# Kernel optimization log

Hardware: AMD Instinct MI355X
Metric: run time of the kernel (lower is better)

The kernel has to match this reference:

```python
import jax, jax.numpy as jnp
import numpy as np

B, N, C_IN = 16, 4096, 64
NPOINT = 1024
RADII = (0.2, 0.4)
NSAMPLES = (32, 64)
MLPS = ((64, 64, 128), (64, 64, 128))
C_TOTAL = sum(m[-1] for m in MLPS)


def setup_inputs() -> dict:
    key = jax.random.key(0)
    ks = jax.random.split(key, 24)
    inp = {
        "xyz": jax.random.uniform(ks[0], (B, N, 3), jnp.float32),
        "features": jax.random.normal(ks[1], (B, N, C_IN), jnp.float32),
        "w_att": jax.random.normal(ks[2], (3 * NPOINT, C_TOTAL), jnp.float32) * 0.02,
        "b_att": jnp.zeros((C_TOTAL,), jnp.float32),
    }
    k = 3
    for g, mlp in enumerate(MLPS):
        cin = 3 + C_IN
        for l, cout in enumerate(mlp):
            inp[f"w{g}_{l}"] = jax.random.normal(ks[k], (cout, cin), jnp.float32) * (1.0 / np.sqrt(cin))
            inp[f"b{g}_{l}"] = jnp.zeros((cout,), jnp.float32)
            k += 1
            cin = cout
    return inp


def _fps(xyz, npoint):
    # furthest point sampling; xyz (B,N,3) -> idx (B,npoint) int32. First idx is 0 (matches CUDA op).
    b, n, _ = xyz.shape
    init_idx = jnp.zeros((b,), jnp.int32)
    init_dist = jnp.full((b, n), 1e10, xyz.dtype)

    def body(carry, _):
        dists, last = carry
        last_pt = jnp.take_along_axis(xyz, last[:, None, None].astype(jnp.int32), axis=1)  # (B,1,3)
        d = jnp.sum((xyz - last_pt) ** 2, axis=-1)  # (B,N)
        dists = jnp.minimum(dists, d)
        nxt = jnp.argmax(dists, axis=-1).astype(jnp.int32)
        return (dists, nxt), nxt

    (_, _), rest = jax.lax.scan(body, (init_dist, init_idx), None, length=npoint - 1)
    return jnp.concatenate([init_idx[None, :], rest], axis=0).T  # (B, npoint)


def _ball_query(radius, nsample, xyz, new_xyz):
    # first-nsample points of xyz within radius of each new_xyz center (slots padded with first hit)
    n = xyz.shape[1]
    d2 = jnp.sum((new_xyz[:, :, None, :] - xyz[:, None, :, :]) ** 2, axis=-1)  # (B,S,N)
    mask = d2 < radius * radius
    order_key = jnp.where(mask, jnp.arange(n, dtype=jnp.int32)[None, None, :], n)
    idx = jnp.argsort(order_key, axis=-1)[..., :nsample].astype(jnp.int32)  # (B,S,nsample)
    valid = jnp.take_along_axis(mask, idx, axis=-1)
    return jnp.where(valid, idx, idx[..., :1])


def _group(xyz, new_xyz, features, idx):
    # -> (B, 3+C, S, nsample): relative xyz concat grouped features
    b, s, ns = idx.shape
    flat = idx.reshape(b, s * ns)
    gx = jnp.take_along_axis(xyz, flat[..., None], axis=1).reshape(b, s, ns, 3)
    gx = gx - new_xyz[:, :, None, :]
    gf = jnp.take_along_axis(features, flat[..., None], axis=1).reshape(b, s, ns, features.shape[-1])
    return jnp.transpose(jnp.concatenate([gx, gf], axis=-1), (0, 3, 1, 2))


def reference(xyz, features, w_att, b_att,
              w0_0, b0_0, w0_1, b0_1, w0_2, b0_2,
              w1_0, b1_0, w1_1, b1_1, w1_2, b1_2):
    xyz_sg = jax.lax.stop_gradient(xyz)  # index selection is non-differentiable (matches CUDA ops)
    fps_idx = _fps(xyz_sg, NPOINT)  # (B, npoint)
    new_xyz = jnp.take_along_axis(xyz, fps_idx[..., None], axis=1)  # (B, npoint, 3)

    # attention gate from sampled coordinates: (B, 3, npoint) flattened -> (B, C_TOTAL)
    att_in = jnp.transpose(new_xyz, (0, 2, 1)).reshape(xyz.shape[0], 3 * NPOINT)
    att = jax.nn.sigmoid(att_in @ w_att + b_att)  # (B, C_TOTAL)

    layer_sets = (((w0_0, b0_0), (w0_1, b0_1), (w0_2, b0_2)),
                  ((w1_0, b1_0), (w1_1, b1_1), (w1_2, b1_2)))
    pooled = []
    new_xyz_sg = jax.lax.stop_gradient(new_xyz)
    for radius, ns, layers in zip(RADII, NSAMPLES, layer_sets):
        idx = _ball_query(radius, ns, xyz_sg, new_xyz_sg)
        x = _group(xyz, new_xyz, features, idx)  # (B, 3+C, S, ns)
        for w, b in layers:  # shared 1x1 conv + ReLU per layer
            x = jax.nn.relu(jnp.einsum('oc,bcsn->bosn', w, x) + b[None, :, None, None])
        pooled.append(jnp.max(x, axis=-1))  # max over nsample -> (B, cout, S)

    features_cat = jnp.concatenate(pooled, axis=1)  # (B, C_TOTAL, S)
    features_end = features_cat * att[:, :, None]
    return new_xyz, features_end
```

## Files before the change

### kernel.cpp

```cpp
#include <hip/hip_runtime.h>
#include <cstdint>
#include <cstddef>


constexpr int B_ = 16, N_ = 4096, S_ = 1024;
constexpr int WT_G = 67*64 + 64*64 + 128*64 + 64 + 64 + 128;
constexpr int WT_BLK = (2*WT_G + 255) / 256;
constexpr int G1_BLK = 2 * B_ * (N_ / 256);

constexpr int WS_XYZF = 0;
constexpr int WS_NXYZ = B_*N_*4;
constexpr int WS_ATT  = WS_NXYZ + B_*S_*3;
constexpr int WS_WT   = WS_ATT + B_*256;
constexpr int WS_IDX0 = WS_WT + 2*WT_G;
constexpr int WS_IDX1 = WS_IDX0 + B_*S_*32;
constexpr int WS_F1   = WS_IDX1 + B_*S_*64;

__global__ __launch_bounds__(256) void g1_kernel(
    const float* __restrict__ xyz, const float* __restrict__ feats,
    const float* __restrict__ w00, const float* __restrict__ w10,
    float* __restrict__ f1) {
  __shared__ float wfs[67 * 64];
  const int fid = blockIdx.x;
  const int g = fid >> 8, b = (fid >> 4) & 15, chunk = fid & 15;
  const float* w = g ? w10 : w00;
  for (int k = threadIdx.x; k < 67*64; k += 256) {
    int c = k >> 6, o = k & 63;
    wfs[k] = w[o*67 + c];
  }
  __syncthreads();
  const int p = chunk * 256 + threadIdx.x;
  const float* xr = xyz + ((size_t)b * N_ + p) * 3;
  const float* fr = feats + ((size_t)b * N_ + p) * 64;
  float acc[64];
  {
    float x0 = xr[0], x1 = xr[1], x2 = xr[2];
#pragma unroll
    for (int j = 0; j < 64; j += 4) {
      float4 wA = *(const float4*)&wfs[0*64 + j];
      acc[j+0] = wA.x * x0; acc[j+1] = wA.y * x0;
      acc[j+2] = wA.z * x0; acc[j+3] = wA.w * x0;
    }
#pragma unroll
    for (int j = 0; j < 64; j += 4) {
      float4 wA = *(const float4*)&wfs[1*64 + j];
      acc[j+0] = fmaf(wA.x, x1, acc[j+0]); acc[j+1] = fmaf(wA.y, x1, acc[j+1]);
      acc[j+2] = fmaf(wA.z, x1, acc[j+2]); acc[j+3] = fmaf(wA.w, x1, acc[j+3]);
    }
#pragma unroll
    for (int j = 0; j < 64; j += 4) {
      float4 wA = *(const float4*)&wfs[2*64 + j];
      acc[j+0] = fmaf(wA.x, x2, acc[j+0]); acc[j+1] = fmaf(wA.y, x2, acc[j+1]);
      acc[j+2] = fmaf(wA.z, x2, acc[j+2]); acc[j+3] = fmaf(wA.w, x2, acc[j+3]);
    }
  }
  for (int c = 0; c < 64; ++c) {
    float v = fr[c];
    const float* wr = &wfs[(3 + c) * 64];
#pragma unroll
    for (int j = 0; j < 64; j += 4) {
      float4 w4 = *(const float4*)&wr[j];
      acc[j+0] = fmaf(w4.x, v, acc[j+0]); acc[j+1] = fmaf(w4.y, v, acc[j+1]);
      acc[j+2] = fmaf(w4.z, v, acc[j+2]); acc[j+3] = fmaf(w4.w, v, acc[j+3]);
    }
  }
  float* op = f1 + (((size_t)g * B_ + b) * N_ + p) * 64;
#pragma unroll
  for (int j = 0; j < 64; j += 4) {
    float4 r = make_float4(acc[j], acc[j+1], acc[j+2], acc[j+3]);
    *(float4*)&op[j] = r;
  }
}

__global__ __launch_bounds__(256) void fps_wt_kernel(
    const float* __restrict__ xyz,
    const float* __restrict__ w00, const float* __restrict__ w01,
    const float* __restrict__ w02, const float* __restrict__ b00,
    const float* __restrict__ b01, const float* __restrict__ b02,
    const float* __restrict__ w10, const float* __restrict__ w11,
    const float* __restrict__ w12, const float* __restrict__ b10,
    const float* __restrict__ b11, const float* __restrict__ b12,
    float4* __restrict__ xyzf, float* __restrict__ wt,
    float* __restrict__ nxyz, float* __restrict__ out_nxyz) {
  constexpr int PPT = 16;
  __shared__ float sx[N_*3];
  __shared__ int   selidx[S_];
  __shared__ alignas(16) unsigned long long redP[2][4];
  __shared__ alignas(16) float4 redC[2][4];

  if (blockIdx.x >= B_) {
    int wid = (blockIdx.x - B_) * 256 + threadIdx.x;
    if (wid >= 2*WT_G) return;
    int g = wid / WT_G, r = wid % WT_G;
    float val;
    if (r < 4288) {
      int c = r >> 6, o = r & 63;
      val = (g ? w10 : w00)[o*67 + c];
    } else if (r < 8384) {
      int rr = r - 4288; int c = rr >> 6, o = rr & 63;
      val = (g ? w11 : w01)[o*64 + c];
    } else if (r < 16576) {
      int rr = r - 8384; int c = rr >> 7, o = rr & 127;
      val = (g ? w12 : w02)[o*64 + c];
    } else {
      int rr = r - 16576;
      val = (rr < 64)  ? (g ? b10 : b00)[rr]
          : (rr < 128) ? (g ? b11 : b01)[rr - 64]
                       : (g ? b12 : b02)[rr - 128];
    }
    wt[g*WT_G + r] = val;
    return;
  }

  const int b = blockIdx.x, t = threadIdx.x;
  const int wv = t >> 6;
  const float* xr = xyz + (size_t)b * N_ * 3;
  for (int k = t; k < N_*3; k += 256) sx[k] = xr[k];
  if (t == 0) selidx[0] = 0;
  __syncthreads();
  float px[PPT], py[PPT], pz[PPT], m[PPT];
#pragma unroll
  for (int p = 0; p < PPT; ++p) {
    int idx = t * PPT + p;
    px[p] = sx[idx*3+0]; py[p] = sx[idx*3+1]; pz[p] = sx[idx*3+2];
    m[p] = 1e10f;
  }
  float lx = sx[0], ly = sx[1], lz = sx[2];
  for (int i = 1; i < S_; ++i) {
#pragma unroll
    for (int p = 0; p < PPT; ++p) {
      float dx = __fsub_rn(px[p], lx), dy = __fsub_rn(py[p], ly), dz = __fsub_rn(pz[p], lz);
      float d = __fadd_rn(__fadd_rn(__fmul_rn(dx,dx), __fmul_rn(dy,dy)), __fmul_rn(dz,dz));
      m[p] = fminf(m[p], d);
    }
    float h0 = fmaxf(fmaxf(m[0],  m[1]),  fmaxf(m[2],  m[3]));
    float h1 = fmaxf(fmaxf(m[4],  m[5]),  fmaxf(m[6],  m[7]));
    float h2 = fmaxf(fmaxf(m[8],  m[9]),  fmaxf(m[10], m[11]));
    float h3 = fmaxf(fmaxf(m[12], m[13]), fmaxf(m[14], m[15]));
    float bv = fmaxf(fmaxf(h0, h1), fmaxf(h2, h3));
    int bp = PPT - 1;
#pragma unroll
    for (int p = PPT - 2; p >= 0; --p)
      if (m[p] == bv) bp = p;
    const int bi = t * PPT + bp;
    unsigned vm = __float_as_uint(bv);
#define DPP_MAX(ctrl) { unsigned o = (unsigned)__builtin_amdgcn_update_dpp((int)vm, (int)vm, (ctrl), 0xf, 0xf, false); vm = vm > o ? vm : o; }
    DPP_MAX(0x111)
    DPP_MAX(0x112)
    DPP_MAX(0x114)
    DPP_MAX(0x118)
    DPP_MAX(0x142)
    DPP_MAX(0x143)
#undef DPP_MAX
    const unsigned wmaxu = (unsigned)__builtin_amdgcn_readlane((int)vm, 63);
    const unsigned long long mk = __ballot(__float_as_uint(bv) == wmaxu);
    const int fl = (int)__builtin_ctzll(mk);
    const int widx = __builtin_amdgcn_readlane(bi, fl);
    const int par = i & 1;
    if (t == (widx >> 4)) {
      const int psel = widx & 15;
      float gx = px[0], gy = py[0], gz = pz[0];
#pragma unroll
      for (int p = 1; p < PPT; ++p)
        if (psel == p) { gx = px[p]; gy = py[p]; gz = pz[p]; }
      redP[par][wv] = ((unsigned long long)wmaxu << 32) | (unsigned)(~widx);
      redC[par][wv] = make_float4(gx, gy, gz, 0.f);
    }
    __syncthreads();
    ulonglong2 pA = *(const ulonglong2*)&redP[par][0];
    ulonglong2 pB = *(const ulonglong2*)&redP[par][2];
    float4 c0 = redC[par][0], c1 = redC[par][1];
    float4 c2 = redC[par][2], c3 = redC[par][3];
    unsigned long long q0 = pA.x > pA.y ? pA.x : pA.y;
    unsigned long long q1 = pB.x > pB.y ? pB.x : pB.y;
    unsigned long long win = q0 > q1 ? q0 : q1;
    const int fi = (int)(~(unsigned)win);
    const int ws = fi >> 10;
    float4 s0 = (ws & 1) ? c1 : c0;
    float4 s1 = (ws & 1) ? c3 : c2;
    float4 fc = (ws & 2) ? s1 : s0;
    lx = fc.x; ly = fc.y; lz = fc.z;
    if (t == 0) selidx[i] = fi;
  }
  __syncthreads();
  for (int k = t; k < S_; k += 256) {
    int id = selidx[k];
    float x = sx[id*3], y = sx[id*3+1], z = sx[id*3+2];
    int o = (b * S_ + k) * 3;
    nxyz[o] = x; nxyz[o+1] = y; nxyz[o+2] = z;
    out_nxyz[o] = x; out_nxyz[o+1] = y; out_nxyz[o+2] = z;
  }
  for (int k = t; k < N_; k += 256) {
    float4 v; v.x = sx[k*3]; v.y = sx[k*3+1]; v.z = sx[k*3+2]; v.w = 0.f;
    xyzf[b * N_ + k] = v;
  }
}

__global__ __launch_bounds__(256) void ballq_att_kernel(
    const float4* __restrict__ xyzf, const float* __restrict__ nxyz,
    int* __restrict__ idx0buf, int* __restrict__ idx1buf,
    const float* __restrict__ w_att, const float* __restrict__ b_att,
    float* __restrict__ att) {
  __shared__ float ai[3 * S_];
  if (blockIdx.x >= B_*S_/4) {
    int b = blockIdx.x - B_*S_/4, t = threadIdx.x;
    for (int k = t; k < 3 * S_; k += 256) {
      int d = k >> 10, s = k & 1023;
      ai[k] = nxyz[(b * S_ + s) * 3 + d];
    }
    __syncthreads();
    float acc = b_att[t];
#pragma unroll 8
    for (int k = 0; k < 3 * S_; ++k)
      acc = fmaf(ai[k], w_att[k * 256 + t], acc);
    att[b * 256 + t] = 1.f / (1.f + expf(-acc));
    return;
  }
  const float r2a = (float)(0.2 * 0.2), r2b = (float)(0.4 * 0.4);
  int lane = threadIdx.x & 63;
  int cid = blockIdx.x * 4 + (threadIdx.x >> 6);
  int b = cid >> 10;
  float cx = nxyz[cid*3], cy = nxyz[cid*3+1], cz = nxyz[cid*3+2];
  const float4* xb = xyzf + b * N_;
  int cnt0 = 0, cnt1 = 0, first0 = 0, first1 = 0;
  const unsigned long long below = (1ull << lane) - 1ull;
  for (int base = 0; base < N_; base += 64) {
    float4 P = xb[base + lane];
    float dx = __fsub_rn(cx, P.x), dy = __fsub_rn(cy, P.y), dz = __fsub_rn(cz, P.z);
    float d2 = __fadd_rn(__fadd_rn(__fmul_rn(dx,dx), __fmul_rn(dy,dy)), __fmul_rn(dz,dz));
    bool h0 = d2 < r2a, h1 = d2 < r2b;
    unsigned long long m0 = __ballot(h0), m1 = __ballot(h1);
    if (cnt0 == 0 && m0 != 0ull) first0 = base + (int)__builtin_ctzll(m0);
    if (cnt1 == 0 && m1 != 0ull) first1 = base + (int)__builtin_ctzll(m1);
    if (h0) {
      int pos = cnt0 + (int)__popcll(m0 & below);
      if (pos < 32) idx0buf[cid * 32 + pos] = base + lane;
    }
    if (h1) {
      int pos = cnt1 + (int)__popcll(m1 & below);
      if (pos < 64) idx1buf[cid * 64 + pos] = base + lane;
    }
    cnt0 += (int)__popcll(m0);
    cnt1 += (int)__popcll(m1);
    if (cnt0 >= 32 && cnt1 >= 64) break;
  }
  if (cnt0 < 32)
    for (int p = cnt0 + lane; p < 32; p += 64) idx0buf[cid * 32 + p] = first0;
  if (cnt1 < 64)
    for (int p = cnt1 + lane; p < 64; p += 64) idx1buf[cid * 64 + p] = first1;
}

template<int NS>
__device__ __forceinline__ void mlp_body(int bi, float* xs, int* pidx,
    float* c1s, const float* __restrict__ f1g,
    const float* __restrict__ nxyz, const float* __restrict__ att,
    const int* __restrict__ idxbuf, const float* __restrict__ wt,
    float* __restrict__ outf, int g) {
  constexpr int NCEN = 128 / NS;
  constexpr int XS = 132;
  float* red = xs;
  const int t = threadIdx.x;
  const int cid0 = bi * NCEN;
  const int b = cid0 >> 10;

  const float* w0  = wt;
  const float* w1  = wt + 67*64;
  const float* w2  = w1 + 64*64;
  const float* bb0 = w2 + 64*128;
  const float* bb1 = bb0 + 64;
  const float* bb2 = bb1 + 64;

  if (t < 128) {
    const int col = t;
    const int cidg = cid0 + col / NS;
    pidx[col] = idxbuf[cidg * NS + (col % NS)];
  }
  if (t < 64 * NCEN) {
    const int o = t & 63, ci = t >> 6;
    const int cid = cid0 + ci;
    float nx = nxyz[cid*3], ny = nxyz[cid*3+1], nz = nxyz[cid*3+2];
    c1s[ci*64 + o] = fmaf(w0[128+o], nz, fmaf(w0[64+o], ny, w0[o]*nx));
  }
  __syncthreads();

  const int og = t & 15, cg = t >> 4;
  float acc[4][8];

  {
    float4 bv = *(const float4*)&bb0[og*4];
    const int ctr = (cg * 8) / NS;
    float4 cv = *(const float4*)&c1s[ctr*64 + og*4];
    float bc[4] = {bv.x - cv.x, bv.y - cv.y, bv.z - cv.z, bv.w - cv.w};
    const int4 pA = *(const int4*)&pidx[cg*8];
    const int4 pB = *(const int4*)&pidx[cg*8 + 4];
    int pc[8] = {pA.x, pA.y, pA.z, pA.w, pB.x, pB.y, pB.z, pB.w};
#pragma unroll
    for (int cc = 0; cc < 8; ++cc) {
      float4 fv = *(const float4*)&f1g[((size_t)b * N_ + pc[cc]) * 64 + og*4];
      acc[0][cc] = bc[0] + fv.x;
      acc[1][cc] = bc[1] + fv.y;
      acc[2][cc] = bc[2] + fv.z;
      acc[3][cc] = bc[3] + fv.w;
    }
  }
#pragma unroll
  for (int oo = 0; oo < 4; ++oo) {
    float4 y0, y1;
    y0.x=fmaxf(acc[oo][0],0.f); y0.y=fmaxf(acc[oo][1],0.f);
    y0.z=fmaxf(acc[oo][2],0.f); y0.w=fmaxf(acc[oo][3],0.f);
    y1.x=fmaxf(acc[oo][4],0.f); y1.y=fmaxf(acc[oo][5],0.f);
    y1.z=fmaxf(acc[oo][6],0.f); y1.w=fmaxf(acc[oo][7],0.f);
    *(float4*)&xs[(og*4+oo)*XS + cg*8]     = y0;
    *(float4*)&xs[(og*4+oo)*XS + cg*8 + 4] = y1;
  }
  __syncthreads();

  {
    float4 bv = *(const float4*)&bb1[og*4];
    float b4[4] = {bv.x, bv.y, bv.z, bv.w};
#pragma unroll
    for (int oo = 0; oo < 4; ++oo)
#pragma unroll
      for (int cc = 0; cc < 8; ++cc) acc[oo][cc] = b4[oo];
    for (int k = 0; k < 64; ++k) {
      float4 x0 = *(const float4*)&xs[k*XS + cg*8];
      float4 x1 = *(const float4*)&xs[k*XS + cg*8 + 4];
      float4 wv = *(const float4*)&w1[k*64 + og*4];
      float x8[8] = {x0.x,x0.y,x0.z,x0.w,x1.x,x1.y,x1.z,x1.w};
      float w4[4] = {wv.x,wv.y,wv.z,wv.w};
#pragma unroll
      for (int oo = 0; oo < 4; ++oo)
#pragma unroll
        for (int cc = 0; cc < 8; ++cc) acc[oo][cc] = fmaf(w4[oo], x8[cc], acc[oo][cc]);
    }
  }
  __syncthreads();
#pragma unroll
  for (int oo = 0; oo < 4; ++oo) {
    float4 y0, y1;
    y0.x=fmaxf(acc[oo][0],0.f); y0.y=fmaxf(acc[oo][1],0.f);
    y0.z=fmaxf(acc[oo][2],0.f); y0.w=fmaxf(acc[oo][3],0.f);
    y1.x=fmaxf(acc[oo][4],0.f); y1.y=fmaxf(acc[oo][5],0.f);
    y1.z=fmaxf(acc[oo][6],0.f); y1.w=fmaxf(acc[oo][7],0.f);
    *(float4*)&xs[(og*4+oo)*XS + cg*8]     = y0;
    *(float4*)&xs[(og*4+oo)*XS + cg*8 + 4] = y1;
  }
  __syncthreads();

  float acc3[8][8];
  {
    float4 b0v = *(const float4*)&bb2[og*8];
    float4 b1v = *(const float4*)&bb2[og*8 + 4];
    float b8[8] = {b0v.x,b0v.y,b0v.z,b0v.w,b1v.x,b1v.y,b1v.z,b1v.w};
#pragma unroll
    for (int oo = 0; oo < 8; ++oo)
#pragma unroll
      for (int cc = 0; cc < 8; ++cc) acc3[oo][cc] = b8[oo];
    for (int k = 0; k < 64; ++k) {
      float4 x0 = *(const float4*)&xs[k*XS + cg*8];
      float4 x1 = *(const float4*)&xs[k*XS + cg*8 + 4];
      float4 wa = *(const float4*)&w2[k*128 + og*8];
      float4 wb = *(const float4*)&w2[k*128 + og*8 + 4];
      float x8[8] = {x0.x,x0.y,x0.z,x0.w,x1.x,x1.y,x1.z,x1.w};
      float w8[8] = {wa.x,wa.y,wa.z,wa.w,wb.x,wb.y,wb.z,wb.w};
#pragma unroll
      for (int oo = 0; oo < 8; ++oo)
#pragma unroll
        for (int cc = 0; cc < 8; ++cc) acc3[oo][cc] = fmaf(w8[oo], x8[cc], acc3[oo][cc]);
    }
  }
  float pm[8];
#pragma unroll
  for (int oo = 0; oo < 8; ++oo) {
    float v = fmaxf(acc3[oo][0], 0.f);
#pragma unroll
    for (int cc = 1; cc < 8; ++cc) v = fmaxf(v, fmaxf(acc3[oo][cc], 0.f));
    pm[oo] = v;
  }
#pragma unroll
  for (int oo = 0; oo < 8; ++oo) {
    pm[oo] = fmaxf(pm[oo], __shfl_xor(pm[oo], 16));
    pm[oo] = fmaxf(pm[oo], __shfl_xor(pm[oo], 32));
  }
  __syncthreads();
  if ((t & 63) < 16) {
    int w = t >> 6;
#pragma unroll
    for (int oo = 0; oo < 8; ++oo) red[w*128 + og*8 + oo] = pm[oo];
  }
  __syncthreads();

  const int ch = t & 127;
  const float a = att[b*256 + g*128 + ch];
  if (NS == 64) {
    int c = t >> 7;
    float v = fmaxf(red[(2*c)*128 + ch], red[(2*c+1)*128 + ch]);
    int s = (cid0 + c) & 1023;
    outf[((size_t)(b*256 + g*128 + ch)) * 1024 + s] = v * a;
  } else {
#pragma unroll
    for (int kk = 0; kk < 2; ++kk) {
      int c = (t >> 7) * 2 + kk;
      float v = red[c*128 + ch];
      int s = (cid0 + c) & 1023;
      outf[((size_t)(b*256 + g*128 + ch)) * 1024 + s] = v * a;
    }
  }
}

__global__ __launch_bounds__(256, 4) void mlp_kernel(
    const float* __restrict__ f1, const float* __restrict__ nxyz,
    const float* __restrict__ att, const int* __restrict__ idx0,
    const int* __restrict__ idx1, const float* __restrict__ wt,
    float* __restrict__ outf) {
  constexpr int XS = 132;
  __shared__ float xs[64 * XS];
  __shared__ int pidx[128];
  __shared__ float c1s[256];
  if (blockIdx.x < 4096)
    mlp_body<32>(blockIdx.x, xs, pidx, c1s, f1, nxyz, att, idx0, wt, outf, 0);
  else
    mlp_body<64>(blockIdx.x - 4096, xs, pidx, c1s, f1 + (size_t)B_*N_*64,
                 nxyz, att, idx1, wt + WT_G, outf, 1);
}

extern "C" void kernel_launch(void* const* d_in, const int* in_sizes, int n_in,
                              void* d_out, int out_size, void* d_ws, size_t ws_size,
                              hipStream_t stream) {
  const float* xyz   = (const float*)d_in[0];
  const float* feats = (const float*)d_in[1];
  const float* w_att = (const float*)d_in[2];
  const float* b_att = (const float*)d_in[3];
  const float* w00 = (const float*)d_in[4];
  const float* b00 = (const float*)d_in[5];
  const float* w01 = (const float*)d_in[6];
  const float* b01 = (const float*)d_in[7];
  const float* w02 = (const float*)d_in[8];
  const float* b02 = (const float*)d_in[9];
  const float* w10 = (const float*)d_in[10];
  const float* b10 = (const float*)d_in[11];
  const float* w11 = (const float*)d_in[12];
  const float* b11 = (const float*)d_in[13];
  const float* w12 = (const float*)d_in[14];
  const float* b12 = (const float*)d_in[15];

  float* wsf = (float*)d_ws;
  int*   wsi = (int*)d_ws;
  float4* xyzf = (float4*)(wsf + WS_XYZF);
  float* nxyz  = wsf + WS_NXYZ;
  float* att   = wsf + WS_ATT;
  float* wt    = wsf + WS_WT;
  int* idx0 = wsi + WS_IDX0;
  int* idx1 = wsi + WS_IDX1;
  float* f1 = wsf + WS_F1;

  float* out  = (float*)d_out;
  float* outf = out + B_ * S_ * 3;

  hipLaunchKernelGGL(g1_kernel, dim3(G1_BLK), dim3(256), 0, stream,
                     xyz, feats, w00, w10, f1);
  hipLaunchKernelGGL(fps_wt_kernel, dim3(B_ + WT_BLK), dim3(256), 0, stream,
                     xyz, w00, w01, w02, b00, b01, b02, w10, w11, w12,
                     b10, b11, b12, xyzf, wt, nxyz, out);
  hipLaunchKernelGGL(ballq_att_kernel, dim3(B_*S_/4 + B_), dim3(256), 0, stream,
                     xyzf, nxyz, idx0, idx1, w_att, b_att, att);
  hipLaunchKernelGGL(mlp_kernel, dim3(12288), dim3(256), 0, stream,
                     f1, nxyz, att, idx0, idx1, wt, outf);
}
```

Baseline: 1.587 ms.

## Process two batches per FPS block to interleave independent serial chains

The furthest point sampling kernel now handles two batch elements per block, with separate shared buffers and register sets, and interleaves their distance updates, DPP reductions and cross-wave reductions so both share one barrier per iteration. The goal is to hide the latency of the serial per-iteration reduction and barrier chain by giving each wave two independent instruction streams. In exchange it doubles register and LDS use per block (about 96KB of shared coordinates) and halves the number of FPS blocks, which lowers parallelism across CUs and may reduce occupancy.

```diff
diff --git a/kernel.cpp b/kernel.cpp
--- a/kernel.cpp
+++ b/kernel.cpp
@@ -7,6 +7,7 @@
 constexpr int WT_G = 67*64 + 64*64 + 128*64 + 64 + 64 + 128;
 constexpr int WT_BLK = (2*WT_G + 255) / 256;
 constexpr int G1_BLK = 2 * B_ * (N_ / 256);
+constexpr int FPB = B_ / 2;
 
 constexpr int WS_XYZF = 0;
 constexpr int WS_NXYZ = B_*N_*4;
@@ -83,13 +84,15 @@
     float4* __restrict__ xyzf, float* __restrict__ wt,
     float* __restrict__ nxyz, float* __restrict__ out_nxyz) {
   constexpr int PPT = 16;
-  __shared__ float sx[N_*3];
-  __shared__ int   selidx[S_];
-  __shared__ alignas(16) unsigned long long redP[2][4];
-  __shared__ alignas(16) float4 redC[2][4];
-
-  if (blockIdx.x >= B_) {
-    int wid = (blockIdx.x - B_) * 256 + threadIdx.x;
+  __shared__ float sxA[N_*3];
+  __shared__ float sxB[N_*3];
+  __shared__ int   selidxA[S_];
+  __shared__ int   selidxB[S_];
+  __shared__ alignas(16) unsigned long long redP[2][2][4];
+  __shared__ alignas(16) float4 redC[2][2][4];
+
+  if (blockIdx.x >= FPB) {
+    int wid = (blockIdx.x - FPB) * 256 + threadIdx.x;
     if (wid >= 2*WT_G) return;
     int g = wid / WT_G, r = wid % WT_G;
     float val;
@@ -112,87 +115,145 @@
     return;
   }
 
-  const int b = blockIdx.x, t = threadIdx.x;
+  const int bA = blockIdx.x, bB = blockIdx.x + FPB, t = threadIdx.x;
   const int wv = t >> 6;
-  const float* xr = xyz + (size_t)b * N_ * 3;
-  for (int k = t; k < N_*3; k += 256) sx[k] = xr[k];
-  if (t == 0) selidx[0] = 0;
-  __syncthreads();
-  float px[PPT], py[PPT], pz[PPT], m[PPT];
+  {
+    const float* xrA = xyz + (size_t)bA * N_ * 3;
+    const float* xrB = xyz + (size_t)bB * N_ * 3;
+    for (int k = t; k < N_*3; k += 256) { sxA[k] = xrA[k]; sxB[k] = xrB[k]; }
+  }
+  if (t == 0) { selidxA[0] = 0; selidxB[0] = 0; }
+  __syncthreads();
+  float pxA[PPT], pyA[PPT], pzA[PPT], mA[PPT];
+  float pxB[PPT], pyB[PPT], pzB[PPT], mB[PPT];
 #pragma unroll
   for (int p = 0; p < PPT; ++p) {
     int idx = t * PPT + p;
-    px[p] = sx[idx*3+0]; py[p] = sx[idx*3+1]; pz[p] = sx[idx*3+2];
-    m[p] = 1e10f;
-  }
-  float lx = sx[0], ly = sx[1], lz = sx[2];
+    pxA[p] = sxA[idx*3+0]; pyA[p] = sxA[idx*3+1]; pzA[p] = sxA[idx*3+2];
+    pxB[p] = sxB[idx*3+0]; pyB[p] = sxB[idx*3+1]; pzB[p] = sxB[idx*3+2];
+    mA[p] = 1e10f; mB[p] = 1e10f;
+  }
+  float lxA = sxA[0], lyA = sxA[1], lzA = sxA[2];
+  float lxB = sxB[0], lyB = sxB[1], lzB = sxB[2];
+
+#define DPP_STEP(v, ctrl) { unsigned o_ = (unsigned)__builtin_amdgcn_update_dpp((int)(v), (int)(v), (ctrl), 0xf, 0xf, false); (v) = (v) > o_ ? (v) : o_; }
+
   for (int i = 1; i < S_; ++i) {
 #pragma unroll
     for (int p = 0; p < PPT; ++p) {
-      float dx = __fsub_rn(px[p], lx), dy = __fsub_rn(py[p], ly), dz = __fsub_rn(pz[p], lz);
+      float dx = __fsub_rn(pxA[p], lxA), dy = __fsub_rn(pyA[p], lyA), dz = __fsub_rn(pzA[p], lzA);
       float d = __fadd_rn(__fadd_rn(__fmul_rn(dx,dx), __fmul_rn(dy,dy)), __fmul_rn(dz,dz));
-      m[p] = fminf(m[p], d);
-    }
-    float h0 = fmaxf(fmaxf(m[0],  m[1]),  fmaxf(m[2],  m[3]));
-    float h1 = fmaxf(fmaxf(m[4],  m[5]),  fmaxf(m[6],  m[7]));
-    float h2 = fmaxf(fmaxf(m[8],  m[9]),  fmaxf(m[10], m[11]));
-    float h3 = fmaxf(fmaxf(m[12], m[13]), fmaxf(m[14], m[15]));
-    float bv = fmaxf(fmaxf(h0, h1), fmaxf(h2, h3));
-    int bp = PPT - 1;
+      mA[p] = fminf(mA[p], d);
+    }
+#pragma unroll
+    for (int p = 0; p < PPT; ++p) {
+      float dx = __fsub_rn(pxB[p], lxB), dy = __fsub_rn(pyB[p], lyB), dz = __fsub_rn(pzB[p], lzB);
+      float d = __fadd_rn(__fadd_rn(__fmul_rn(dx,dx), __fmul_rn(dy,dy)), __fmul_rn(dz,dz));
+      mB[p] = fminf(mB[p], d);
+    }
+    float hA0 = fmaxf(fmaxf(mA[0],  mA[1]),  fmaxf(mA[2],  mA[3]));
+    float hA1 = fmaxf(fmaxf(mA[4],  mA[5]),  fmaxf(mA[6],  mA[7]));
+    float hA2 = fmaxf(fmaxf(mA[8],  mA[9]),  fmaxf(mA[10], mA[11]));
+    float hA3 = fmaxf(fmaxf(mA[12], mA[13]), fmaxf(mA[14], mA[15]));
+    float bvA = fmaxf(fmaxf(hA0, hA1), fmaxf(hA2, hA3));
+    int bpA = PPT - 1;
 #pragma unroll
     for (int p = PPT - 2; p >= 0; --p)
-      if (m[p] == bv) bp = p;
-    const int bi = t * PPT + bp;
-    unsigned vm = __float_as_uint(bv);
-#define DPP_MAX(ctrl) { unsigned o = (unsigned)__builtin_amdgcn_update_dpp((int)vm, (int)vm, (ctrl), 0xf, 0xf, false); vm = vm > o ? vm : o; }
-    DPP_MAX(0x111)
-    DPP_MAX(0x112)
-    DPP_MAX(0x114)
-    DPP_MAX(0x118)
-    DPP_MAX(0x142)
-    DPP_MAX(0x143)
-#undef DPP_MAX
-    const unsigned wmaxu = (unsigned)__builtin_amdgcn_readlane((int)vm, 63);
-    const unsigned long long mk = __ballot(__float_as_uint(bv) == wmaxu);
-    const int fl = (int)__builtin_ctzll(mk);
-    const int widx = __builtin_amdgcn_readlane(bi, fl);
+      if (mA[p] == bvA) bpA = p;
+    const int biA = t * PPT + bpA;
+    float hB0 = fmaxf(fmaxf(mB[0],  mB[1]),  fmaxf(mB[2],  mB[3]));
+    float hB1 = fmaxf(fmaxf(mB[4],  mB[5]),  fmaxf(mB[6],  mB[7]));
+    float hB2 = fmaxf(fmaxf(mB[8],  mB[9]),  fmaxf(mB[10], mB[11]));
+    float hB3 = fmaxf(fmaxf(mB[12], mB[13]), fmaxf(mB[14], mB[15]));
+    float bvB = fmaxf(fmaxf(hB0, hB1), fmaxf(hB2, hB3));
+    int bpB = PPT - 1;
+#pragma unroll
+    for (int p = PPT - 2; p >= 0; --p)
+      if (mB[p] == bvB) bpB = p;
+    const int biB = t * PPT + bpB;
+    unsigned vmA = __float_as_uint(bvA);
+    unsigned vmB = __float_as_uint(bvB);
+    DPP_STEP(vmA, 0x111) DPP_STEP(vmB, 0x111)
+    DPP_STEP(vmA, 0x112) DPP_STEP(vmB, 0x112)
+    DPP_STEP(vmA, 0x114) DPP_STEP(vmB, 0x114)
+    DPP_STEP(vmA, 0x118) DPP_STEP(vmB, 0x118)
+    DPP_STEP(vmA, 0x142) DPP_STEP(vmB, 0x142)
+    DPP_STEP(vmA, 0x143) DPP_STEP(vmB, 0x143)
+    const unsigned wmaxuA = (unsigned)__builtin_amdgcn_readlane((int)vmA, 63);
+    const unsigned wmaxuB = (unsigned)__builtin_amdgcn_readlane((int)vmB, 63);
+    const unsigned long long mkA = __ballot(__float_as_uint(bvA) == wmaxuA);
+    const unsigned long long mkB = __ballot(__float_as_uint(bvB) == wmaxuB);
+    const int flA = (int)__builtin_ctzll(mkA);
+    const int flB = (int)__builtin_ctzll(mkB);
+    const int widxA = __builtin_amdgcn_readlane(biA, flA);
+    const int widxB = __builtin_amdgcn_readlane(biB, flB);
     const int par = i & 1;
-    if (t == (widx >> 4)) {
-      const int psel = widx & 15;
-      float gx = px[0], gy = py[0], gz = pz[0];
+    if (t == (widxA >> 4)) {
+      const int psel = widxA & 15;
+      float gx = pxA[0], gy = pyA[0], gz = pzA[0];
 #pragma unroll
       for (int p = 1; p < PPT; ++p)
-        if (psel == p) { gx = px[p]; gy = py[p]; gz = pz[p]; }
-      redP[par][wv] = ((unsigned long long)wmaxu << 32) | (unsigned)(~widx);
-      redC[par][wv] = make_float4(gx, gy, gz, 0.f);
+        if (psel == p) { gx = pxA[p]; gy = pyA[p]; gz = pzA[p]; }
+      redP[0][par][wv] = ((unsigned long long)wmaxuA << 32) | (unsigned)(~widxA);
+      redC[0][par][wv] = make_float4(gx, gy, gz, 0.f);
+    }
+    if (t == (widxB >> 4)) {
+      const int psel = widxB & 15;
+      float gx = pxB[0], gy = pyB[0], gz = pzB[0];
+#pragma unroll
+      for (int p = 1; p < PPT; ++p)
+        if (psel == p) { gx = pxB[p]; gy = pyB[p]; gz = pzB[p]; }
+      redP[1][par][wv] = ((unsigned long long)wmaxuB << 32) | (unsigned)(~widxB);
+      redC[1][par][wv] = make_float4(gx, gy, gz, 0.f);
     }
     __syncthreads();
-    ulonglong2 pA = *(const ulonglong2*)&redP[par][0];
-    ulonglong2 pB = *(const ulonglong2*)&redP[par][2];
-    float4 c0 = redC[par][0], c1 = redC[par][1];
-    float4 c2 = redC[par][2], c3 = redC[par][3];
-    unsigned long long q0 = pA.x > pA.y ? pA.x : pA.y;
-    unsigned long long q1 = pB.x > pB.y ? pB.x : pB.y;
-    unsigned long long win = q0 > q1 ? q0 : q1;
-    const int fi = (int)(~(unsigned)win);
-    const int ws = fi >> 10;
-    float4 s0 = (ws & 1) ? c1 : c0;
-    float4 s1 = (ws & 1) ? c3 : c2;
-    float4 fc = (ws & 2) ? s1 : s0;
-    lx = fc.x; ly = fc.y; lz = fc.z;
-    if (t == 0) selidx[i] = fi;
-  }
+    ulonglong2 pA0 = *(const ulonglong2*)&redP[0][par][0];
+    ulonglong2 pA1 = *(const ulonglong2*)&redP[0][par][2];
+    ulonglong2 pB0 = *(const ulonglong2*)&redP[1][par][0];
+    ulonglong2 pB1 = *(const ulonglong2*)&redP[1][par][2];
+    float4 cA0 = redC[0][par][0], cA1 = redC[0][par][1];
+    float4 cA2 = redC[0][par][2], cA3 = redC[0][par][3];
+    float4 cB0 = redC[1][par][0], cB1 = redC[1][par][1];
+    float4 cB2 = redC[1][par][2], cB3 = redC[1][par][3];
+    unsigned long long qA0 = pA0.x > pA0.y ? pA0.x : pA0.y;
+    unsigned long long qA1 = pA1.x > pA1.y ? pA1.x : pA1.y;
+    unsigned long long winA = qA0 > qA1 ? qA0 : qA1;
+    unsigned long long qB0 = pB0.x > pB0.y ? pB0.x : pB0.y;
+    unsigned long long qB1 = pB1.x > pB1.y ? pB1.x : pB1.y;
+    unsigned long long winB = qB0 > qB1 ? qB0 : qB1;
+    const int fiA = (int)(~(unsigned)winA);
+    const int fiB = (int)(~(unsigned)winB);
+    const int wsA = fiA >> 10;
+    const int wsB = fiB >> 10;
+    float4 sA0 = (wsA & 1) ? cA1 : cA0;
+    float4 sA1 = (wsA & 1) ? cA3 : cA2;
+    float4 fcA = (wsA & 2) ? sA1 : sA0;
+    float4 sB0 = (wsB & 1) ? cB1 : cB0;
+    float4 sB1 = (wsB & 1) ? cB3 : cB2;
+    float4 fcB = (wsB & 2) ? sB1 : sB0;
+    lxA = fcA.x; lyA = fcA.y; lzA = fcA.z;
+    lxB = fcB.x; lyB = fcB.y; lzB = fcB.z;
+    if (t == 0) { selidxA[i] = fiA; selidxB[i] = fiB; }
+  }
+#undef DPP_STEP
   __syncthreads();
   for (int k = t; k < S_; k += 256) {
-    int id = selidx[k];
-    float x = sx[id*3], y = sx[id*3+1], z = sx[id*3+2];
-    int o = (b * S_ + k) * 3;
-    nxyz[o] = x; nxyz[o+1] = y; nxyz[o+2] = z;
-    out_nxyz[o] = x; out_nxyz[o+1] = y; out_nxyz[o+2] = z;
+    int idA = selidxA[k];
+    float xA = sxA[idA*3], yA = sxA[idA*3+1], zA = sxA[idA*3+2];
+    int oA = (bA * S_ + k) * 3;
+    nxyz[oA] = xA; nxyz[oA+1] = yA; nxyz[oA+2] = zA;
+    out_nxyz[oA] = xA; out_nxyz[oA+1] = yA; out_nxyz[oA+2] = zA;
+    int idB = selidxB[k];
+    float xB = sxB[idB*3], yB = sxB[idB*3+1], zB = sxB[idB*3+2];
+    int oB = (bB * S_ + k) * 3;
+    nxyz[oB] = xB; nxyz[oB+1] = yB; nxyz[oB+2] = zB;
+    out_nxyz[oB] = xB; out_nxyz[oB+1] = yB; out_nxyz[oB+2] = zB;
   }
   for (int k = t; k < N_; k += 256) {
-    float4 v; v.x = sx[k*3]; v.y = sx[k*3+1]; v.z = sx[k*3+2]; v.w = 0.f;
-    xyzf[b * N_ + k] = v;
+    float4 vA; vA.x = sxA[k*3]; vA.y = sxA[k*3+1]; vA.z = sxA[k*3+2]; vA.w = 0.f;
+    xyzf[bA * N_ + k] = vA;
+    float4 vB; vB.x = sxB[k*3]; vB.y = sxB[k*3+1]; vB.z = sxB[k*3+2]; vB.w = 0.f;
+    xyzf[bB * N_ + k] = vB;
   }
 }
 
@@ -459,7 +520,7 @@
 
   hipLaunchKernelGGL(g1_kernel, dim3(G1_BLK), dim3(256), 0, stream,
                      xyz, feats, w00, w10, f1);
-  hipLaunchKernelGGL(fps_wt_kernel, dim3(B_ + WT_BLK), dim3(256), 0, stream,
+  hipLaunchKernelGGL(fps_wt_kernel, dim3(FPB + WT_BLK), dim3(256), 0, stream,
                      xyz, w00, w01, w02, b00, b01, b02, w10, w11, w12,
                      b10, b11, b12, xyzf, wt, nxyz, out);
   hipLaunchKernelGGL(ballq_att_kernel, dim3(B_*S_/4 + B_), dim3(256), 0, stream,
```

Result: slower. 2.394 ms (+50.8%).
